# Optimization experiments

Measured on AMD Instinct MI355X. Metric: run time of the kernel, lower is better.

## Reference

```python
import jax, jax.numpy as jnp
import numpy as np

B, T, V, D, H, L = 8, 1024, 8192, 768, 12, 6
DH = D // H
FF = 4 * D
EPS = 1e-5


def setup_inputs() -> dict:
    key = jax.random.key(0)
    ks = jax.random.split(key, 12)
    s = 0.02
    return {
        "idx": jax.random.randint(ks[0], (B, T), 0, V),
        "targets": jax.random.randint(ks[1], (B, T), 0, V),
        "tok_emb": jax.random.normal(ks[2], (V, D), jnp.float32) * s,
        "pos_emb": jax.random.normal(ks[3], (T, D), jnp.float32) * s,
        "ln1_g": jnp.ones((L, D), jnp.float32),
        "ln1_b": jnp.zeros((L, D), jnp.float32),
        "Wq": jax.random.normal(ks[4], (L, H, D, DH), jnp.float32) * s,
        "Wk": jax.random.normal(ks[5], (L, H, D, DH), jnp.float32) * s,
        "Wv": jax.random.normal(ks[6], (L, H, D, DH), jnp.float32) * s,
        "Wproj": jax.random.normal(ks[7], (L, D, D), jnp.float32) * s,
        "bproj": jnp.zeros((L, D), jnp.float32),
        "ln2_g": jnp.ones((L, D), jnp.float32),
        "ln2_b": jnp.zeros((L, D), jnp.float32),
        "W1": jax.random.normal(ks[8], (L, D, FF), jnp.float32) * s,
        "b1": jnp.zeros((L, FF), jnp.float32),
        "W2": jax.random.normal(ks[9], (L, FF, D), jnp.float32) * s,
        "b2": jnp.zeros((L, D), jnp.float32),
        "lnf_g": jnp.ones((D,), jnp.float32),
        "lnf_b": jnp.zeros((D,), jnp.float32),
        "W_lm": jax.random.normal(ks[10], (D, V), jnp.float32) * s,
        "b_lm": jnp.zeros((V,), jnp.float32),
    }


def _ln(x, g, b):
    m = jnp.mean(x, axis=-1, keepdims=True)
    v = jnp.var(x, axis=-1, keepdims=True)
    return (x - m) * jax.lax.rsqrt(v + EPS) * g + b


def reference(idx, targets, tok_emb, pos_emb, ln1_g, ln1_b, Wq, Wk, Wv, Wproj,
              bproj, ln2_g, ln2_b, W1, b1, W2, b2, lnf_g, lnf_b, W_lm, b_lm):
    b, t = idx.shape
    x = tok_emb[idx] + pos_emb[:t]  # [B,T,D]
    mask = jnp.tril(jnp.ones((t, t), bool))
    scale = D ** -0.5  # NOTE: original scales by n_embd**-0.5, not head_size**-0.5

    def step(x, p):
        g1, bb1_, wq, wk, wv, wp, bp, g2, bb2_, w1, bia1, w2, bia2 = p
        h = _ln(x, g1, bb1_)
        q = jnp.einsum('btd,hde->bhte', h, wq)  # [B,H,T,DH]
        k = jnp.einsum('btd,hde->bhte', h, wk)
        v = jnp.einsum('btd,hde->bhte', h, wv)
        scores = jnp.einsum('bhqe,bhke->bhqk', q, k) * scale
        scores = jnp.where(mask, scores, -jnp.inf)
        w = jax.nn.softmax(scores, axis=-1)
        o = jnp.einsum('bhqk,bhke->bhqe', w, v)
        o = o.transpose(0, 2, 1, 3).reshape(b, t, D)  # concat heads
        x = x + o @ wp + bp
        h2 = _ln(x, g2, bb2_)
        x = x + jax.nn.relu(h2 @ w1 + bia1) @ w2 + bia2
        return x, None

    x, _ = jax.lax.scan(step, x, (ln1_g, ln1_b, Wq, Wk, Wv, Wproj, bproj,
                                  ln2_g, ln2_b, W1, b1, W2, b2))
    x = _ln(x, lnf_g, lnf_b)
    logits = x @ W_lm + b_lm  # [B,T,V]
    logp = jax.nn.log_softmax(logits, axis=-1)
    loss = -jnp.take_along_axis(logp, targets[..., None], axis=-1).mean()
    return logits, loss
```

## Files before the change

kernel.cpp:

```cpp
#include <hip/hip_runtime.h>
#include <hip/hip_bf16.h>

typedef unsigned int uint;
typedef unsigned short ushort;

typedef short s16x8 __attribute__((ext_vector_type(8)));
typedef ushort u16x4 __attribute__((ext_vector_type(4)));
typedef float f32x4 __attribute__((ext_vector_type(4)));
typedef uint  u32x4 __attribute__((ext_vector_type(4)));

#define NB 8
#define NT 1024
#define NV 8192
#define ND 768
#define NH 12
#define NL 6
#define NDH 64
#define NFF 3072
#define NTOK (NB*NT)

__device__ __forceinline__ ushort f2bf(float f) {
  uint x = __float_as_uint(f);
  x += 0x7FFFu + ((x >> 16) & 1u);
  return (ushort)(x >> 16);
}
__device__ __forceinline__ float bf2f(ushort u) {
  return __uint_as_float(((uint)u) << 16);
}

__device__ __forceinline__ int swz(int row, int col) {
  return row * 64 + ((((col >> 3) ^ row) & 7) << 3) + (col & 7);
}

__device__ __forceinline__ void gload16(const ushort* g, ushort* l) {
  __builtin_amdgcn_global_load_lds(
      (const __attribute__((address_space(1))) void*)g,
      (__attribute__((address_space(3))) void*)l, 16, 0, 0);
}

__global__ __launch_bounds__(192) void embed_kernel(
    const int* __restrict__ idx, const float* __restrict__ tok,
    const float* __restrict__ pos, ushort* __restrict__ x)
{
  int n = blockIdx.x, t = threadIdx.x;
  int token = idx[n];
  const float4* tp = (const float4*)(tok + (size_t)token * ND);
  const float4* pp = (const float4*)(pos + (size_t)(n & (NT - 1)) * ND);
  float4 a = tp[t], b = pp[t];
  u16x4 r;
  r.x = f2bf(a.x + b.x); r.y = f2bf(a.y + b.y);
  r.z = f2bf(a.z + b.z); r.w = f2bf(a.w + b.w);
  *(u16x4*)&x[(size_t)n * ND + t * 4] = r;
}

__global__ __launch_bounds__(192) void ln_kernel(
    const ushort* __restrict__ x, const float* __restrict__ g,
    const float* __restrict__ b, ushort* __restrict__ out)
{
  int row = blockIdx.x, tid = threadIdx.x;
  const ushort* xr = x + (size_t)row * ND;
  u16x4 xv = *(const u16x4*)&xr[tid * 4];
  float v0 = bf2f(xv.x), v1 = bf2f(xv.y), v2 = bf2f(xv.z), v3 = bf2f(xv.w);
  float s = v0 + v1 + v2 + v3;
  float q = v0 * v0 + v1 * v1 + v2 * v2 + v3 * v3;
  #pragma unroll
  for (int d = 1; d < 64; d <<= 1) { s += __shfl_xor(s, d); q += __shfl_xor(q, d); }
  __shared__ float rs[3], rq[3];
  int w = tid >> 6;
  if ((tid & 63) == 0) { rs[w] = s; rq[w] = q; }
  __syncthreads();
  s = rs[0] + rs[1] + rs[2];
  q = rq[0] + rq[1] + rq[2];
  float mean = s * (1.0f / ND);
  float inv = rsqrtf(q * (1.0f / ND) - mean * mean + 1e-5f);
  float4 gv = *(const float4*)&g[tid * 4];
  float4 bv = *(const float4*)&b[tid * 4];
  u16x4 o;
  o.x = f2bf((v0 - mean) * inv * gv.x + bv.x);
  o.y = f2bf((v1 - mean) * inv * gv.y + bv.y);
  o.z = f2bf((v2 - mean) * inv * gv.z + bv.z);
  o.w = f2bf((v3 - mean) * inv * gv.w + bv.w);
  *(u16x4*)&out[(size_t)row * ND + tid * 4] = o;
}

__device__ __forceinline__ void transp_body(
    ushort (*t)[72], const float* __restrict__ in, ushort* __restrict__ out,
    int R, int C, int HB, size_t sh, size_t sl, int bid)
{
  const int tid = threadIdx.x;
  int ntx = C >> 6, nty = R >> 6;
  int tpb = ntx * nty;
  int bi = bid / tpb;
  int rem = bid - bi * tpb;
  int ty = rem / ntx, tx = rem - ty * ntx;
  int r0 = ty << 6, c0 = tx << 6;
  const float* ip = in + (size_t)bi * R * C;
  #pragma unroll
  for (int p = 0; p < 4; ++p) {
    int r = (tid >> 4) + p * 16;
    int c = (tid & 15) * 4;
    float4 v = *(const float4*)&ip[(size_t)(r0 + r) * C + c0 + c];
    t[c + 0][r] = f2bf(v.x); t[c + 1][r] = f2bf(v.y);
    t[c + 2][r] = f2bf(v.z); t[c + 3][r] = f2bf(v.w);
  }
  __syncthreads();
  ushort* op = out + (size_t)(bi / HB) * sl + (size_t)(bi % HB) * sh;
  #pragma unroll
  for (int p = 0; p < 4; ++p) {
    int c = (tid >> 4) + p * 16;
    int r = (tid & 15) * 4;
    u16x4 o = *(const u16x4*)&t[c][r];
    *(u16x4*)&op[(size_t)(c0 + c) * R + r0 + r] = o;
  }
}

__global__ __launch_bounds__(256) void transp_all(
    const float* __restrict__ Wq, const float* __restrict__ Wk,
    const float* __restrict__ Wv, const float* __restrict__ Wp,
    const float* __restrict__ W1, const float* __restrict__ W2,
    const float* __restrict__ Wlm,
    ushort* __restrict__ qkvT, ushort* __restrict__ wpT,
    ushort* __restrict__ w1T, ushort* __restrict__ w2T,
    ushort* __restrict__ wlmT)
{
  __shared__ ushort t[64][72];
  const size_t LQKV = (size_t)2304 * ND;
  const size_t SH = (size_t)NDH * ND;
  int bid = blockIdx.x;
  if (bid < 864)        transp_body(t, Wq, qkvT,                    ND, NDH, NH, SH, LQKV, bid);
  else if (bid < 1728)  transp_body(t, Wk, qkvT + (size_t)ND*ND,    ND, NDH, NH, SH, LQKV, bid - 864);
  else if (bid < 2592)  transp_body(t, Wv, qkvT + (size_t)2*ND*ND,  ND, NDH, NH, SH, LQKV, bid - 1728);
  else if (bid < 3456)  transp_body(t, Wp, wpT, ND, ND, 1, 0, (size_t)ND * ND, bid - 2592);
  else if (bid < 6912)  transp_body(t, W1, w1T, ND, NFF, 1, 0, (size_t)ND * NFF, bid - 3456);
  else if (bid < 10368) transp_body(t, W2, w2T, NFF, ND, 1, 0, (size_t)ND * NFF, bid - 6912);
  else                  transp_body(t, Wlm, wlmT, ND, NV, 1, 0, (size_t)ND * NV, bid - 10368);
}

template<bool BIAS, bool RELU, bool RESID, int OUT>
__global__ __launch_bounds__(256) void gemm_bt(
    const ushort* __restrict__ A, const ushort* __restrict__ Bt,
    const float* __restrict__ bias, ushort* __restrict__ xres,
    void* __restrict__ outp, void* __restrict__ outp2,
    int M, int N, int K)
{
  __shared__ ushort As[8192];
  __shared__ ushort Bs[8192];
  const int tid = threadIdx.x;
  const int lane = tid & 63;
  const int w = tid >> 6;
  const int wr = w >> 1, wc = w & 1;
  const int lg = lane >> 4, li = lane & 15;
  const int m0 = blockIdx.y * 128, n0 = blockIdx.x * 128;

  const int tr = tid >> 3;
  const int tc = ((tid & 7) ^ (tr & 7)) << 3;
  const ushort* gA = &A[(size_t)(m0 + tr) * K + tc];
  const ushort* gB = &Bt[(size_t)(n0 + tr) * K + tc];

  f32x4 acc[4][4];
  #pragma unroll
  for (int i = 0; i < 4; ++i)
    #pragma unroll
    for (int j = 0; j < 4; ++j) { f32x4 z = {0.f,0.f,0.f,0.f}; acc[i][j] = z; }

  for (int kk = 0; kk < K; kk += 64) {
    __syncthreads();
    #pragma unroll
    for (int g = 0; g < 4; ++g) {
      gload16(gA + (size_t)(g * 32) * K + kk, &As[g * 2048 + w * 512]);
      gload16(gB + (size_t)(g * 32) * K + kk, &Bs[g * 2048 + w * 512]);
    }
    __syncthreads();
    #pragma unroll
    for (int kh = 0; kh < 2; ++kh) {
      s16x8 af[4], bfr[4];
      #pragma unroll
      for (int i = 0; i < 4; ++i) {
        int ra = wr * 64 + i * 16 + li;
        int rb = wc * 64 + i * 16 + li;
        int cha = (((kh * 4 + lg) ^ (ra & 7)) << 3);
        int chb = (((kh * 4 + lg) ^ (rb & 7)) << 3);
        af[i]  = *(const s16x8*)&As[ra * 64 + cha];
        bfr[i] = *(const s16x8*)&Bs[rb * 64 + chb];
      }
      #pragma unroll
      for (int i = 0; i < 4; ++i)
        #pragma unroll
        for (int j = 0; j < 4; ++j)
          acc[i][j] = __builtin_amdgcn_mfma_f32_16x16x32_bf16(af[i], bfr[j], acc[i][j], 0, 0, 0);
    }
  }

  #pragma unroll
  for (int i = 0; i < 4; ++i) {
    #pragma unroll
    for (int j = 0; j < 4; ++j) {
      int row0 = m0 + wr * 64 + i * 16 + lg * 4;
      int col  = n0 + wc * 64 + j * 16 + li;
      float bv = BIAS ? bias[col] : 0.f;
      #pragma unroll
      for (int ii = 0; ii < 4; ++ii) {
        float val = acc[i][j][ii] + bv;
        if (RELU) val = fmaxf(val, 0.f);
        size_t off = (size_t)(row0 + ii) * N + col;
        if (RESID) { val += bf2f(xres[off]); xres[off] = f2bf(val); }
        if (OUT == 1) ((ushort*)outp)[off] = f2bf(val);
      }
    }
  }
}

template<bool BIAS, bool RELU, int OUT>
__global__ __launch_bounds__(512) void gemm_wide(
    const ushort* __restrict__ A, const ushort* __restrict__ Bt,
    const float* __restrict__ bias,
    void* __restrict__ outp, void* __restrict__ outp2,
    int M, int N, int K)
{
  __shared__ ushort As[8192];
  __shared__ ushort Bs[16384];
  const int tid = threadIdx.x;
  const int lane = tid & 63;
  const int w = tid >> 6;
  const int wr = w >> 2, wc = w & 3;
  const int lg = lane >> 4, li = lane & 15;
  const int m0 = blockIdx.y * 128, n0 = blockIdx.x * 256;

  const int lr = lane >> 3;
  const int lc = ((lane & 7) ^ lr) << 3;
  const ushort* gA = &A[(size_t)(m0 + w * 8 + lr) * K + lc];
  const ushort* gB = &Bt[(size_t)(n0 + w * 8 + lr) * K + lc];

  f32x4 acc[4][4];
  #pragma unroll
  for (int i = 0; i < 4; ++i)
    #pragma unroll
    for (int j = 0; j < 4; ++j) { f32x4 z = {0.f,0.f,0.f,0.f}; acc[i][j] = z; }

  for (int kk = 0; kk < K; kk += 64) {
    __syncthreads();
    #pragma unroll
    for (int g = 0; g < 2; ++g)
      gload16(gA + (size_t)(g * 64) * K + kk, &As[(g * 64 + w * 8) * 64]);
    #pragma unroll
    for (int g = 0; g < 4; ++g)
      gload16(gB + (size_t)(g * 64) * K + kk, &Bs[(g * 64 + w * 8) * 64]);
    __syncthreads();
    #pragma unroll
    for (int kh = 0; kh < 2; ++kh) {
      s16x8 af[4], bfr[4];
      #pragma unroll
      for (int i = 0; i < 4; ++i) {
        int ra = wr * 64 + i * 16 + li;
        int rb = wc * 64 + i * 16 + li;
        int cha = (((kh * 4 + lg) ^ (ra & 7)) << 3);
        int chb = (((kh * 4 + lg) ^ (rb & 7)) << 3);
        af[i]  = *(const s16x8*)&As[ra * 64 + cha];
        bfr[i] = *(const s16x8*)&Bs[rb * 64 + chb];
      }
      #pragma unroll
      for (int i = 0; i < 4; ++i)
        #pragma unroll
        for (int j = 0; j < 4; ++j)
          acc[i][j] = __builtin_amdgcn_mfma_f32_16x16x32_bf16(af[i], bfr[j], acc[i][j], 0, 0, 0);
    }
  }

  if (OUT == 2) {
    float2* pstat = (float2*)outp2;
    float* op = (float*)outp;
    float bvv[4];
    #pragma unroll
    for (int j = 0; j < 4; ++j)
      bvv[j] = BIAS ? bias[n0 + wc * 64 + j * 16 + li] : 0.f;
    #pragma unroll
    for (int i = 0; i < 4; ++i) {
      #pragma unroll
      for (int ii = 0; ii < 4; ++ii) {
        int row = m0 + wr * 64 + i * 16 + lg * 4 + ii;
        float v4[4];
        float mx = -1e30f;
        #pragma unroll
        for (int j = 0; j < 4; ++j) {
          float val = acc[i][j][ii] + bvv[j];
          op[(size_t)row * N + n0 + wc * 64 + j * 16 + li] = val;
          v4[j] = val; mx = fmaxf(mx, val);
        }
        #pragma unroll
        for (int d = 1; d < 16; d <<= 1) mx = fmaxf(mx, __shfl_xor(mx, d));
        float se = 0.f;
        #pragma unroll
        for (int j = 0; j < 4; ++j) se += __expf(v4[j] - mx);
        #pragma unroll
        for (int d = 1; d < 16; d <<= 1) se += __shfl_xor(se, d);
        if (li == 0) {
          float2 pv; pv.x = mx; pv.y = se;
          pstat[(size_t)row * 128 + (n0 >> 6) + wc] = pv;
        }
      }
    }
    return;
  }

  const bool isV = (OUT == 3) && (n0 >= 1536);
  #pragma unroll
  for (int i = 0; i < 4; ++i) {
    #pragma unroll
    for (int j = 0; j < 4; ++j) {
      int row0 = m0 + wr * 64 + i * 16 + lg * 4;
      int col  = n0 + wc * 64 + j * 16 + li;
      float bv = BIAS ? bias[col] : 0.f;
      if (isV) {
        int dhg = col - 1536;
        int hh = dhg >> 6, dh = dhg & 63;
        int b_ = row0 >> 10, t0 = row0 & (NT - 1);
        u16x4 o;
        o.x = f2bf(acc[i][j][0]); o.y = f2bf(acc[i][j][1]);
        o.z = f2bf(acc[i][j][2]); o.w = f2bf(acc[i][j][3]);
        *(u16x4*)&((ushort*)outp2)[((size_t)(b_ * NH + hh) * 64 + dh) * NT + t0] = o;
      } else {
        #pragma unroll
        for (int ii = 0; ii < 4; ++ii) {
          float val = acc[i][j][ii] + bv;
          if (RELU) val = fmaxf(val, 0.f);
          size_t off = (size_t)(row0 + ii) * N + col;
          ((ushort*)outp)[off] = f2bf(val);
        }
      }
    }
  }
}

__global__ __launch_bounds__(256) void attn_kernel(
    const ushort* __restrict__ qkv, const ushort* __restrict__ vT,
    ushort* __restrict__ o)
{
  __shared__ ushort Ks[64 * 64];
  __shared__ ushort Vt[64 * 64];
  __shared__ ushort Ps[4][32 * 64];

  const int tid = threadIdx.x;
  const int lane = tid & 63;
  const int w = tid >> 6;
  const int lg = lane >> 4;
  const int li = lane & 15;

  int bid = blockIdx.x;
  const int qt = bid & 7;
  const int h = (bid >> 3) % NH;
  const int b = bid / (8 * NH);
  const int q0 = qt * 128 + w * 32;
  const size_t nbase = (size_t)b * NT;
  const int hq = h * NDH;
  const int hk = ND + h * NDH;

  s16x8 aq[2][2];
  #pragma unroll
  for (int f = 0; f < 2; ++f)
    #pragma unroll
    for (int c = 0; c < 2; ++c)
      aq[f][c] = *(const s16x8*)&qkv[(nbase + q0 + f * 16 + li) * (3 * ND) + hq + c * 32 + lg * 8];

  float m_r[2][4], l_r[2][4];
  f32x4 oacc[2][4];
  #pragma unroll
  for (int f = 0; f < 2; ++f)
    #pragma unroll
    for (int i = 0; i < 4; ++i) { m_r[f][i] = -1e30f; l_r[f][i] = 0.f; }
  #pragma unroll
  for (int f = 0; f < 2; ++f)
    #pragma unroll
    for (int n = 0; n < 4; ++n) { f32x4 z = {0.f,0.f,0.f,0.f}; oacc[f][n] = z; }

  const float scale = 0.036084391824351615f;
  const ushort* vTb = vT + (size_t)(b * NH + h) * 64 * NT;

  const int nkc = 2 * qt + 2;
  for (int kc = 0; kc < nkc; ++kc) {
    {
      const int kr = lane >> 3;
      const int ch = lane & 7;
      #pragma unroll
      for (int g = 0; g < 2; ++g) {
        int row = g * 32 + w * 8 + kr;
        gload16(&qkv[(nbase + kc * 64 + row) * (size_t)(3 * ND) + hk + ((ch ^ (row & 7)) << 3)],
                &Ks[(g * 32 + w * 8) * 64]);
        gload16(&vTb[(size_t)row * NT + kc * 64 + ((ch ^ (row & 7)) << 3)],
                &Vt[(g * 32 + w * 8) * 64]);
      }
    }
    __syncthreads();
    if (kc * 64 <= q0 + 31) {
      f32x4 s[2][4];
      #pragma unroll
      for (int kt = 0; kt < 4; ++kt) {
        s16x8 bk[2];
        #pragma unroll
        for (int c = 0; c < 2; ++c)
          bk[c] = *(const s16x8*)&Ks[swz(kt * 16 + li, c * 32 + lg * 8)];
        #pragma unroll
        for (int f = 0; f < 2; ++f) {
          f32x4 z = {0.f,0.f,0.f,0.f}; s[f][kt] = z;
          #pragma unroll
          for (int c = 0; c < 2; ++c)
            s[f][kt] = __builtin_amdgcn_mfma_f32_16x16x32_bf16(aq[f][c], bk[c], s[f][kt], 0, 0, 0);
        }
      }
      #pragma unroll
      for (int f = 0; f < 2; ++f) {
        #pragma unroll
        for (int i = 0; i < 4; ++i) {
          int row = q0 + f * 16 + lg * 4 + i;
          float sv[4]; float mx = -1e30f;
          #pragma unroll
          for (int kt = 0; kt < 4; ++kt) {
            int key = kc * 64 + kt * 16 + li;
            float t = s[f][kt][i] * scale;
            t = (key <= row) ? t : -1e30f;
            sv[kt] = t; mx = fmaxf(mx, t);
          }
          #pragma unroll
          for (int d = 1; d < 16; d <<= 1) mx = fmaxf(mx, __shfl_xor(mx, d));
          float mnew = fmaxf(m_r[f][i], mx);
          float corr = __expf(m_r[f][i] - mnew);
          float ps = 0.f;
          #pragma unroll
          for (int kt = 0; kt < 4; ++kt) {
            float pe = __expf(sv[kt] - mnew);
            ps += pe;
            Ps[w][swz(f * 16 + lg * 4 + i, kt * 16 + li)] = f2bf(pe);
          }
          #pragma unroll
          for (int d = 1; d < 16; d <<= 1) ps += __shfl_xor(ps, d);
          l_r[f][i] = l_r[f][i] * corr + ps;
          m_r[f][i] = mnew;
          #pragma unroll
          for (int n = 0; n < 4; ++n) oacc[f][n][i] *= corr;
        }
      }
      #pragma unroll
      for (int c = 0; c < 2; ++c) {
        s16x8 ap[2], bv[4];
        #pragma unroll
        for (int f = 0; f < 2; ++f)
          ap[f] = *(const s16x8*)&Ps[w][swz(f * 16 + li, c * 32 + lg * 8)];
        #pragma unroll
        for (int n = 0; n < 4; ++n)
          bv[n] = *(const s16x8*)&Vt[swz(n * 16 + li, c * 32 + lg * 8)];
        #pragma unroll
        for (int f = 0; f < 2; ++f)
          #pragma unroll
          for (int n = 0; n < 4; ++n)
            oacc[f][n] = __builtin_amdgcn_mfma_f32_16x16x32_bf16(ap[f], bv[n], oacc[f][n], 0, 0, 0);
      }
    }
    __syncthreads();
  }
  #pragma unroll
  for (int f = 0; f < 2; ++f)
    #pragma unroll
    for (int n = 0; n < 4; ++n)
      #pragma unroll
      for (int i = 0; i < 4; ++i) {
        float val = oacc[f][n][i] / l_r[f][i];
        o[(nbase + q0 + f * 16 + lg * 4 + i) * ND + hq + n * 16 + li] = f2bf(val);
      }
}

__global__ __launch_bounds__(128) void loss_lse(
    const float2* __restrict__ pstat, const float* __restrict__ logits,
    const int* __restrict__ targets, float* __restrict__ rowloss)
{
  int row = blockIdx.x, tid = threadIdx.x;
  float2 p = pstat[(size_t)row * 128 + tid];
  float mx = p.x;
  #pragma unroll
  for (int d = 1; d < 64; d <<= 1) mx = fmaxf(mx, __shfl_xor(mx, d));
  __shared__ float sm[2], ss[2];
  int w = tid >> 6;
  if ((tid & 63) == 0) sm[w] = mx;
  __syncthreads();
  mx = fmaxf(sm[0], sm[1]);
  float se = p.y * __expf(p.x - mx);
  #pragma unroll
  for (int d = 1; d < 64; d <<= 1) se += __shfl_xor(se, d);
  if ((tid & 63) == 0) ss[w] = se;
  __syncthreads();
  if (tid == 0) {
    float lse = mx + __logf(ss[0] + ss[1]);
    rowloss[row] = lse - logits[(size_t)row * NV + targets[row]];
  }
}

__global__ __launch_bounds__(256) void loss_reduce(
    const float* __restrict__ rowloss, float* __restrict__ out_loss)
{
  int tid = threadIdx.x;
  float s = 0.f;
  #pragma unroll
  for (int i = 0; i < 32; ++i) s += rowloss[tid + i * 256];
  #pragma unroll
  for (int d = 1; d < 64; d <<= 1) s += __shfl_xor(s, d);
  __shared__ float red[4];
  int w = tid >> 6, lane = tid & 63;
  if (lane == 0) red[w] = s;
  __syncthreads();
  if (tid == 0) {
    float total = red[0] + red[1] + red[2] + red[3];
    out_loss[0] = total * (1.0f / NTOK);
  }
}

extern "C" void kernel_launch(void* const* d_in, const int* in_sizes, int n_in,
                              void* d_out, int out_size, void* d_ws, size_t ws_size,
                              hipStream_t stream)
{
  const int*   idx     = (const int*)d_in[0];
  const int*   targets = (const int*)d_in[1];
  const float* tok     = (const float*)d_in[2];
  const float* pos     = (const float*)d_in[3];
  const float* ln1g    = (const float*)d_in[4];
  const float* ln1b    = (const float*)d_in[5];
  const float* Wq      = (const float*)d_in[6];
  const float* Wk      = (const float*)d_in[7];
  const float* Wv      = (const float*)d_in[8];
  const float* Wp      = (const float*)d_in[9];
  const float* bp      = (const float*)d_in[10];
  const float* ln2g    = (const float*)d_in[11];
  const float* ln2b    = (const float*)d_in[12];
  const float* W1      = (const float*)d_in[13];
  const float* b1      = (const float*)d_in[14];
  const float* W2      = (const float*)d_in[15];
  const float* b2      = (const float*)d_in[16];
  const float* lnfg    = (const float*)d_in[17];
  const float* lnfb    = (const float*)d_in[18];
  const float* Wlm     = (const float*)d_in[19];
  const float* blm     = (const float*)d_in[20];

  char* ob = (char*)d_out;
  ushort* x    = (ushort*)ob;
  ushort* qkvb = (ushort*)(ob + 25165824);
  ushort* mid  = (ushort*)(ob + 25165824);
  ushort* qkvT = (ushort*)(ob + 75497472);
  ushort* wpT  = (ushort*)(ob + 75497472 + 21233664);
  ushort* w1T  = (ushort*)(ob + 75497472 + 28311552);
  ushort* w2T  = (ushort*)(ob + 75497472 + 56623104);
  ushort* vTb  = (ushort*)(ob + 160432128);
  float* logits = (float*)d_out;

  char* ws = (char*)d_ws;
  size_t off = 0;
  auto alloc = [&](size_t bytes) -> void* {
    void* p = ws + off; off += (bytes + 255) & ~(size_t)255; return p;
  };
  ushort* h    = (ushort*)alloc((size_t)NTOK * ND * 2);
  ushort* wlmT = (ushort*)alloc((size_t)ND * NV * 2);
  float*  rowloss = (float*)alloc((size_t)NTOK * 4);
  float*  pstat = (float*)alloc((size_t)NTOK * 128 * 8);

  embed_kernel<<<NTOK, 192, 0, stream>>>(idx, tok, pos, x);

  transp_all<<<11904, 256, 0, stream>>>(Wq, Wk, Wv, Wp, W1, W2, Wlm,
                                        qkvT, wpT, w1T, w2T, wlmT);

  const size_t LQKV = (size_t)2304 * ND;
  dim3 gqkv(2304 / 256, NTOK / 128);
  dim3 g768(ND / 128, NTOK / 128);
  dim3 gff(NFF / 256, NTOK / 128);
  dim3 glm(NV / 256, NTOK / 128);

  for (int l = 0; l < NL; ++l) {
    ln_kernel<<<NTOK, 192, 0, stream>>>(x, ln1g + l * ND, ln1b + l * ND, h);
    gemm_wide<false,false,3><<<gqkv, 512, 0, stream>>>(h, qkvT + l * LQKV, nullptr, qkvb, vTb, NTOK, 2304, ND);
    attn_kernel<<<NB * NH * (NT / 128), 256, 0, stream>>>(qkvb, vTb, h);
    gemm_bt<true,false,true,0><<<g768, 256, 0, stream>>>(h, wpT + (size_t)l * ND * ND, bp + l * ND, x, nullptr, nullptr, NTOK, ND, ND);
    ln_kernel<<<NTOK, 192, 0, stream>>>(x, ln2g + l * ND, ln2b + l * ND, h);
    gemm_wide<true,true,1><<<gff, 512, 0, stream>>>(h, w1T + (size_t)l * ND * NFF, b1 + (size_t)l * NFF, mid, nullptr, NTOK, NFF, ND);
    gemm_bt<true,false,true,0><<<g768, 256, 0, stream>>>(mid, w2T + (size_t)l * ND * NFF, b2 + l * ND, x, nullptr, nullptr, NTOK, ND, NFF);
  }

  ln_kernel<<<NTOK, 192, 0, stream>>>(x, lnfg, lnfb, h);
  gemm_wide<true,false,2><<<glm, 512, 0, stream>>>(h, wlmT, blm, logits, pstat, NTOK, NV, ND);

  loss_lse<<<NTOK, 128, 0, stream>>>((const float2*)pstat, logits, targets, rowloss);
  loss_reduce<<<1, 256, 0, stream>>>(rowloss, logits + (size_t)NTOK * NV);
}
```

Baseline: 2.114 ms.

## Double-buffer K/V tiles in attention kernel to overlap loads with compute

Splits the attention kernel's shared K and V tiles into two ping-pong buffers. The next chunk is prefetched with direct-to-LDS loads while the current chunk's QK^T, softmax and PV run. The loop is unrolled by two, and __syncthreads is replaced with an explicit vmcnt wait plus s_barrier. This hides global load latency at the cost of doubling K/V LDS use, which may reduce occupancy.

```diff
diff --git a/kernel.cpp b/kernel.cpp
--- a/kernel.cpp
+++ b/kernel.cpp
@@ -335,8 +335,10 @@
     const ushort* __restrict__ qkv, const ushort* __restrict__ vT,
     ushort* __restrict__ o)
 {
-  __shared__ ushort Ks[64 * 64];
-  __shared__ ushort Vt[64 * 64];
+  __shared__ ushort Ks0[64 * 64];
+  __shared__ ushort Ks1[64 * 64];
+  __shared__ ushort Vt0[64 * 64];
+  __shared__ ushort Vt1[64 * 64];
   __shared__ ushort Ps[4][32 * 64];
 
   const int tid = threadIdx.x;
@@ -374,36 +376,42 @@
 
   const float scale = 0.036084391824351615f;
   const ushort* vTb = vT + (size_t)(b * NH + h) * 64 * NT;
-
-  const int nkc = 2 * qt + 2;
-  for (int kc = 0; kc < nkc; ++kc) {
-    {
-      const int kr = lane >> 3;
-      const int ch = lane & 7;
-      #pragma unroll
-      for (int g = 0; g < 2; ++g) {
-        int row = g * 32 + w * 8 + kr;
-        gload16(&qkv[(nbase + kc * 64 + row) * (size_t)(3 * ND) + hk + ((ch ^ (row & 7)) << 3)],
-                &Ks[(g * 32 + w * 8) * 64]);
-        gload16(&vTb[(size_t)row * NT + kc * 64 + ((ch ^ (row & 7)) << 3)],
-                &Vt[(g * 32 + w * 8) * 64]);
-      }
-    }
-    __syncthreads();
-    if (kc * 64 <= q0 + 31) {
+  const int kr = lane >> 3;
+  const int ch = lane & 7;
+
+  auto STAGE = [&](int kc_, ushort* kd, ushort* vd) {
+    #pragma unroll
+    for (int g = 0; g < 2; ++g) {
+      int row = g * 32 + w * 8 + kr;
+      gload16(&qkv[(nbase + kc_ * 64 + row) * (size_t)(3 * ND) + hk + ((ch ^ (row & 7)) << 3)],
+              &kd[(g * 32 + w * 8) * 64]);
+      gload16(&vTb[(size_t)row * NT + kc_ * 64 + ((ch ^ (row & 7)) << 3)],
+              &vd[(g * 32 + w * 8) * 64]);
+    }
+  };
+
+  auto BODY = [&](int kc, const ushort* Kb, const ushort* Vb,
+                  ushort* Kn, ushort* Vn, bool stage_next) {
+    const bool comp = (kc * 64 <= q0 + 31);
+    s16x8 bk[4][2];
+    if (comp) {
+      #pragma unroll
+      for (int kt = 0; kt < 4; ++kt)
+        #pragma unroll
+        for (int c = 0; c < 2; ++c)
+          bk[kt][c] = *(const s16x8*)&Kb[swz(kt * 16 + li, c * 32 + lg * 8)];
+    }
+    if (stage_next) STAGE(kc + 1, Kn, Vn);
+    if (comp) {
       f32x4 s[2][4];
       #pragma unroll
       for (int kt = 0; kt < 4; ++kt) {
-        s16x8 bk[2];
-        #pragma unroll
-        for (int c = 0; c < 2; ++c)
-          bk[c] = *(const s16x8*)&Ks[swz(kt * 16 + li, c * 32 + lg * 8)];
         #pragma unroll
         for (int f = 0; f < 2; ++f) {
           f32x4 z = {0.f,0.f,0.f,0.f}; s[f][kt] = z;
           #pragma unroll
           for (int c = 0; c < 2; ++c)
-            s[f][kt] = __builtin_amdgcn_mfma_f32_16x16x32_bf16(aq[f][c], bk[c], s[f][kt], 0, 0, 0);
+            s[f][kt] = __builtin_amdgcn_mfma_f32_16x16x32_bf16(aq[f][c], bk[kt][c], s[f][kt], 0, 0, 0);
         }
       }
       #pragma unroll
@@ -446,7 +454,7 @@
           ap[f] = *(const s16x8*)&Ps[w][swz(f * 16 + li, c * 32 + lg * 8)];
         #pragma unroll
         for (int n = 0; n < 4; ++n)
-          bv[n] = *(const s16x8*)&Vt[swz(n * 16 + li, c * 32 + lg * 8)];
+          bv[n] = *(const s16x8*)&Vb[swz(n * 16 + li, c * 32 + lg * 8)];
         #pragma unroll
         for (int f = 0; f < 2; ++f)
           #pragma unroll
@@ -454,8 +462,19 @@
             oacc[f][n] = __builtin_amdgcn_mfma_f32_16x16x32_bf16(ap[f], bv[n], oacc[f][n], 0, 0, 0);
       }
     }
-    __syncthreads();
-  }
+    asm volatile("s_waitcnt vmcnt(0)" ::: "memory");
+    asm volatile("s_barrier" ::: "memory");
+  };
+
+  const int nkc = 2 * qt + 2;
+  STAGE(0, Ks0, Vt0);
+  asm volatile("s_waitcnt vmcnt(0)" ::: "memory");
+  asm volatile("s_barrier" ::: "memory");
+  for (int kc = 0; kc < nkc; kc += 2) {
+    BODY(kc,     Ks0, Vt0, Ks1, Vt1, kc + 1 < nkc);
+    BODY(kc + 1, Ks1, Vt1, Ks0, Vt0, kc + 2 < nkc);
+  }
+
   #pragma unroll
   for (int f = 0; f < 2; ++f)
     #pragma unroll
```

Result: slower. 2.168 ms (+2.6%).
